# Kernel tuning notes

Hardware: AMD Instinct MI355X
Metric: run time of the kernel (lower is better)

Reference implementation:

```python
import jax, jax.numpy as jnp
import numpy as np

B, N, C = 32, 128, 128
HE = 64                      # n_hidden_edge
FILTERS = [64, 256, 512]
K = 3
NREL = 2
NH = 256                     # n_hidden
OUT = 10
EPS_BN = 1e-5


def _lin(key, fin, fout):
    return jax.random.normal(key, (fin, fout), jnp.float32) / np.sqrt(fin)


def setup_inputs() -> dict:
    key = jax.random.key(0)
    ks = iter(jax.random.split(key, 64))
    x = jax.random.normal(next(ks), (B, N, C), jnp.float32)
    # ragged mask: first n_b nodes active
    n_nodes = jax.random.randint(next(ks), (B,), 64, N + 1)
    mask = (jnp.arange(N)[None, :] < n_nodes[:, None]).astype(jnp.float32)
    A = jax.random.uniform(next(ks), (B, N, N), jnp.float32)
    A = A * mask[:, :, None] * mask[:, None, :]
    inp = {"x": x, "A": A, "mask": mask}
    # edge predictor MLP: Linear(2C,HE) -> ReLU -> Linear(HE,1)
    inp["eW1"] = _lin(next(ks), 2 * C, HE)
    inp["eb1"] = jnp.zeros((HE,), jnp.float32)
    inp["eW2"] = _lin(next(ks), HE, 1)
    inp["eb2"] = jnp.zeros((1,), jnp.float32)
    # 3 GraphConv layers: fc (in*K*NREL -> f), BN eval params
    fin = C
    for li, f in enumerate(FILTERS):
        inp[f"gW{li}"] = _lin(next(ks), fin * K * NREL, f)
        inp[f"gb{li}"] = jnp.zeros((f,), jnp.float32)
        inp[f"g{li}g"] = jnp.ones((f,), jnp.float32)
        inp[f"g{li}b"] = jnp.zeros((f,), jnp.float32)
        inp[f"g{li}m"] = 0.1 * jax.random.normal(next(ks), (f,), jnp.float32)
        inp[f"g{li}v"] = jax.random.uniform(next(ks), (f,), jnp.float32) + 0.5
        fin = f
    # classifier fc (dropout is identity in eval)
    inp["fW1"] = _lin(next(ks), FILTERS[-1], NH)
    inp["fb1"] = jnp.zeros((NH,), jnp.float32)
    inp["fW2"] = _lin(next(ks), NH, OUT)
    inp["fb2"] = jnp.zeros((OUT,), jnp.float32)
    return inp


def _edge_adjacency(x, mask, eW1, eb1, eW2, eb2):
    # edge_pred(cat(x_i,x_j)) for all pairs; flipped pass == transpose of scores
    u = x @ eW1[:C]          # [B,N,HE] (contribution of node i slot)
    v = x @ eW1[C:]          # [B,N,HE] (contribution of node j slot)
    h = jax.nn.relu(u[:, :, None, :] + v[:, None, :, :] + eb1)   # [B,N,N,HE]
    s = jnp.einsum('bijh,h->bij', h, eW2[:, 0]) + eb2[0]          # [B,N,N]
    y = jnp.exp(0.5 * (s + jnp.swapaxes(s, 1, 2)))
    # only masked upper-triangular pairs (i<j) were scattered in the original
    tri = jnp.triu(jnp.ones((N, N), bool), 1)
    pm = tri[None, :, :] * (mask[:, :, None] * mask[:, None, :])
    A_pred = y * pm
    rs = jnp.sum(A_pred, axis=2)                                 # row sums (torch sum over dim 1 of [N,N])
    rs = jnp.where(rs == 0.0, 1.0, rs)
    An = A_pred / rs[:, :, None]
    return An + jnp.swapaxes(An, 1, 2)


def _gconv(xh, A2, mask, W, b, g, be, m, v):
    outs = []
    for rel in range(A2.shape[-1]):
        Ar = A2[..., rel]
        # K>=2, scale_identity=False -> no identity added
        D = (jnp.sum(Ar, axis=1) + 1e-5) ** (-0.5)               # [B,N]
        L = D[:, :, None] * Ar * D[:, None, :]
        Xt = [xh, jnp.matmul(L, xh)]
        for _ in range(2, K):
            Xt.append(2.0 * jnp.matmul(L, Xt[-1]) - Xt[-2])
        outs.append(jnp.concatenate(Xt, axis=2))
    h = jnp.concatenate(outs, axis=2) @ W + b
    h = h * mask[:, :, None]
    h = (h - m) / jnp.sqrt(v + EPS_BN) * g + be                  # BatchNorm1d eval over channel dim
    return jax.nn.relu(h)


def reference(x, A, mask, eW1, eb1, eW2, eb2,
              gW0, gb0, g0g, g0b, g0m, g0v,
              gW1, gb1, g1g, g1b, g1m, g1v,
              gW2, gb2, g2g, g2b, g2m, g2v,
              fW1, fb1, fW2, fb2):
    An = _edge_adjacency(x, mask, eW1, eb1, eW2, eb2)
    A2 = jnp.stack((A, An), axis=3)                              # [B,N,N,2]
    h = _gconv(x, A2, mask, gW0, gb0, g0g, g0b, g0m, g0v)
    h = _gconv(h, A2, mask, gW1, gb1, g1g, g1b, g1m, g1v)
    h = _gconv(h, A2, mask, gW2, gb2, g2g, g2b, g2m, g2v)
    pooled = jnp.max(h, axis=1)                                  # [B, 512]
    # fc: Dropout(eval=id) -> Linear -> Dropout(eval=id) -> Linear (no activation)
    return (pooled @ fW1 + fb1) @ fW2 + fb2
```

## Files before the change

kernel.cpp:

```cpp
#include <hip/hip_runtime.h>

#define Bk 32
#define Nn 128
#define Cc 128
#define HE 64
#define BN_EPS 1e-5f

typedef __attribute__((ext_vector_type(8))) short short8;
typedef __attribute__((ext_vector_type(4))) float floatx4;

#define OFF_UV   ((size_t)0)
#define OFF_AP   ((size_t)524288)
#define OFF_LB   ((size_t)1048576)
#define OFF_H0   ((size_t)1572864)
#define OFF_H1   ((size_t)1835008)
#define OFF_POOL ((size_t)2883584)
#define OFF_WC   ((size_t)2899968)
#define OFF_BC   ((size_t)2905088)
#define OFF_XB0  ((size_t)2905104)
#define OFF_XB   ((size_t)3167248)
#define OFF_WT   ((size_t)6312976)
#define WUV_OFS  933888

__device__ __forceinline__ unsigned short f2b(float f) {
    unsigned int x = __float_as_uint(f);
    unsigned int r = x + 0x7FFFu + ((x >> 16) & 1u);
    return (unsigned short)(r >> 16);
}

__global__ __launch_bounds__(256) void prep_all(const float* __restrict__ W0,
                                                const float* __restrict__ W1,
                                                const float* __restrict__ W2,
                                                const float* __restrict__ eW1,
                                                const float* __restrict__ fW1,
                                                const float* __restrict__ fb1,
                                                const float* __restrict__ fW2,
                                                const float* __restrict__ fb2,
                                                const float* __restrict__ x,
                                                unsigned short* __restrict__ Wt,
                                                float* __restrict__ Wc,
                                                float* __restrict__ bc,
                                                unsigned short* __restrict__ xb0) {
    __shared__ unsigned short Ts[64][65];
    int bid = blockIdx.x, tid = threadIdx.x;
    if (bid < 228) {
        const float* src; unsigned short* dst; int N, ldK, k0, n0;
        if (bid < 12)      { src = W0; dst = Wt;          N = 64;  ldK = 768;  k0 = bid * 64;        n0 = 0; }
        else if (bid < 36) { int t = bid - 12; src = W1; dst = Wt + 49152;  N = 256; ldK = 384;  k0 = (t % 6) * 64;  n0 = (t / 6) * 64; }
        else               { int t = bid - 36; src = W2; dst = Wt + 147456; N = 512; ldK = 1536; k0 = (t % 24) * 64; n0 = (t / 24) * 64; }
#pragma unroll
        for (int p = 0; p < 16; ++p) {
            int e = tid + p * 256; int r = e >> 6, c = e & 63;
            Ts[r][c] = f2b(src[(size_t)(k0 + r) * N + n0 + c]);
        }
        __syncthreads();
#pragma unroll
        for (int p = 0; p < 16; ++p) {
            int e = tid + p * 256; int n = e >> 6, k = e & 63;
            dst[(size_t)(n0 + n) * ldK + k0 + k] = Ts[k][n];
        }
        return;
    }
    if (bid < 232) {
        int tt = bid - 228;
        int half = tt >> 1, kt = tt & 1;
        int k0 = kt * 64;
        unsigned short* Wuv = Wt + WUV_OFS;
#pragma unroll
        for (int p = 0; p < 16; ++p) {
            int e = tid + p * 256; int r = e >> 6, c = e & 63;
            Ts[r][c] = f2b(eW1[(size_t)(half * 128 + k0 + r) * 64 + c]);
        }
        __syncthreads();
#pragma unroll
        for (int p = 0; p < 16; ++p) {
            int e = tid + p * 256; int n = e >> 6, k = e & 63;
            Wuv[(size_t)(half * 64 + n) * 128 + k0 + k] = Ts[k][n];
        }
        return;
    }
    if (bid < 253) {
        int e = (bid - 232) * 256 + tid;
        if (e < 5120) {
            int i = e / 10, j = e - i * 10;
            float acc = 0.f;
            for (int h = 0; h < 256; ++h) acc += fW1[(size_t)i * 256 + h] * fW2[(size_t)h * 10 + j];
            Wc[e] = acc;
        } else if (e < 5130) {
            int j = e - 5120;
            float acc = fb2[j];
            for (int h = 0; h < 256; ++h) acc += fb1[h] * fW2[(size_t)h * 10 + j];
            bc[j] = acc;
        }
        return;
    }
    {
        int idx = (bid - 253) * 256 + tid;
        float4 vv = ((const float4*)x)[idx];
        ushort4 o;
        o.x = f2b(vv.x); o.y = f2b(vv.y); o.z = f2b(vv.z); o.w = f2b(vv.w);
        ((ushort4*)xb0)[idx] = o;
    }
}

__global__ __launch_bounds__(256) void uv_mfma(const unsigned short* __restrict__ xb0,
                                               const unsigned short* __restrict__ Wuv,
                                               const float* __restrict__ eb1,
                                               float* __restrict__ uv) {
    __shared__ __align__(16) unsigned short As[128 * 40];
    __shared__ __align__(16) unsigned short Bs[64 * 40];
    int tid = threadIdx.x;
    int w = tid >> 6, lane = tid & 63, quad = lane >> 4, lr = lane & 15;
    int row0 = blockIdx.y * 128, col0 = blockIdx.x * 64;
    floatx4 acc[2][4];
#pragma unroll
    for (int rt = 0; rt < 2; ++rt)
#pragma unroll
        for (int ct = 0; ct < 4; ++ct) acc[rt][ct] = (floatx4){0.f, 0.f, 0.f, 0.f};
    int arow[2], asub[2];
#pragma unroll
    for (int i = 0; i < 2; ++i) { int ch = tid + i * 256; arow[i] = ch >> 2; asub[i] = ch & 3; }
    int brow = tid >> 2, bsub = tid & 3;
    for (int k0 = 0; k0 < 128; k0 += 32) {
        short8 ra[2];
#pragma unroll
        for (int i = 0; i < 2; ++i)
            ra[i] = *(const short8*)(xb0 + (size_t)(row0 + arow[i]) * 128 + k0 + asub[i] * 8);
        short8 rb = *(const short8*)(Wuv + (size_t)(col0 + brow) * 128 + k0 + bsub * 8);
        __syncthreads();
#pragma unroll
        for (int i = 0; i < 2; ++i) *(short8*)&As[arow[i] * 40 + asub[i] * 8] = ra[i];
        *(short8*)&Bs[brow * 40 + bsub * 8] = rb;
        __syncthreads();
        short8 a[2], b[4];
#pragma unroll
        for (int rt = 0; rt < 2; ++rt)
            a[rt] = *(const short8*)&As[(w * 32 + rt * 16 + lr) * 40 + quad * 8];
#pragma unroll
        for (int ct = 0; ct < 4; ++ct)
            b[ct] = *(const short8*)&Bs[(ct * 16 + lr) * 40 + quad * 8];
#pragma unroll
        for (int rt = 0; rt < 2; ++rt)
#pragma unroll
            for (int ct = 0; ct < 4; ++ct)
                acc[rt][ct] = __builtin_amdgcn_mfma_f32_16x16x32_bf16(a[rt], b[ct], acc[rt][ct], 0, 0, 0);
    }
#pragma unroll
    for (int rt = 0; rt < 2; ++rt) {
        int rbase = row0 + w * 32 + rt * 16 + quad * 4;
#pragma unroll
        for (int ct = 0; ct < 4; ++ct) {
            int col = col0 + ct * 16 + lr;
            float bi = (col < 64) ? eb1[col] : 0.f;
#pragma unroll
            for (int reg = 0; reg < 4; ++reg)
                uv[(size_t)(rbase + reg) * 128 + col] = acc[rt][ct][reg] + bi;
        }
    }
}

__global__ __launch_bounds__(256) void edge_sym(const float* __restrict__ uv,
                                                const float* __restrict__ eW2,
                                                const float* __restrict__ eb2,
                                                const float* __restrict__ mask,
                                                float* __restrict__ ap) {
    __shared__ __align__(16) float ui[16][68], vi[16][68], uj[16][68], vj[16][68];
    __shared__ __align__(16) float w2[64];
    int t = blockIdx.x, b = blockIdx.y;
    int ti = 0, rem = t;
    for (;;) { int w = 8 - ti; if (rem < w) break; rem -= w; ++ti; }
    int tj = ti + rem;
    int i0 = ti * 16, j0 = tj * 16;
    int tid = threadIdx.x;
    int r = tid >> 4, c4 = (tid & 15) * 4;
    const float* uvb = uv + (size_t)b * Nn * 128;
    *(float4*)&ui[r][c4] = *(const float4*)(uvb + (size_t)(i0 + r) * 128 + c4);
    *(float4*)&vi[r][c4] = *(const float4*)(uvb + (size_t)(i0 + r) * 128 + 64 + c4);
    *(float4*)&uj[r][c4] = *(const float4*)(uvb + (size_t)(j0 + r) * 128 + c4);
    *(float4*)&vj[r][c4] = *(const float4*)(uvb + (size_t)(j0 + r) * 128 + 64 + c4);
    if (tid < 64) w2[tid] = eW2[tid];
    __syncthreads();
    int il = tid >> 4, jl = tid & 15;
    int gi = i0 + il, gj = j0 + jl;
    if (gj <= gi) return;
    float d = 0.f;
#pragma unroll
    for (int h4 = 0; h4 < 16; ++h4) {
        float4 a1 = *(const float4*)&ui[il][h4 * 4];
        float4 b1 = *(const float4*)&vj[jl][h4 * 4];
        float4 a2 = *(const float4*)&uj[jl][h4 * 4];
        float4 b2 = *(const float4*)&vi[il][h4 * 4];
        float4 ww = *(const float4*)&w2[h4 * 4];
        d += (fmaxf(a1.x + b1.x, 0.f) + fmaxf(a2.x + b2.x, 0.f)) * ww.x
           + (fmaxf(a1.y + b1.y, 0.f) + fmaxf(a2.y + b2.y, 0.f)) * ww.y
           + (fmaxf(a1.z + b1.z, 0.f) + fmaxf(a2.z + b2.z, 0.f)) * ww.z
           + (fmaxf(a1.w + b1.w, 0.f) + fmaxf(a2.w + b2.w, 0.f)) * ww.w;
    }
    float p = 0.5f * d + eb2[0];
    float mi = mask[b * Nn + gi], mj = mask[b * Nn + gj];
    float val = (mi != 0.f && mj != 0.f) ? expf(fminf(p, 80.f)) : 0.f;
    ap[((size_t)(b * Nn + gi)) * Nn + gj] = val;
}

__global__ __launch_bounds__(256) void adj_L(const float* __restrict__ ap,
                                             const float* __restrict__ A,
                                             unsigned short* __restrict__ Lb) {
    int bid = blockIdx.x, tid = threadIdx.x;
    if (bid < 32) {
        int b = bid;
        __shared__ float apS[128][129];
        __shared__ float part[256], invS[128], t1S[128], Dv[128];
        const float* apg = ap + (size_t)b * Nn * Nn;
        for (int k = 0; k < 64; ++k) {
            int idx = tid + k * 256;
            int i = idx >> 7, j = idx & 127;
            float g = apg[idx];
            apS[i][j] = (j > i) ? g : 0.f;
        }
        __syncthreads();
        {
            int row = tid >> 1, half = tid & 1;
            float s0 = 0.f;
            for (int j = half * 64; j < half * 64 + 64; ++j) s0 += apS[row][j];
            part[tid] = s0;
        }
        __syncthreads();
        if (tid < 128) {
            float rsum = part[tid * 2] + part[tid * 2 + 1];
            invS[tid] = (rsum == 0.f) ? 1.f : (1.f / rsum);
            t1S[tid]  = (rsum == 0.f) ? 0.f : 1.f;
        }
        __syncthreads();
        {
            int col = tid >> 1, half = tid & 1;
            float s0 = 0.f;
            for (int j = half * 64; j < half * 64 + 64; ++j) s0 += apS[j][col] * invS[j];
            part[tid] = s0;
        }
        __syncthreads();
        if (tid < 128) Dv[tid] = rsqrtf(t1S[tid] + part[tid * 2] + part[tid * 2 + 1] + 1e-5f);
        __syncthreads();
        unsigned short* Lo = Lb + ((size_t)(Bk + b)) * Nn * Nn;
        for (int k = 0; k < 64; ++k) {
            int idx = tid + k * 256;
            int i = idx >> 7, j = idx & 127;
            float an = apS[i][j] * invS[i] + apS[j][i] * invS[j];
            Lo[idx] = f2b(Dv[i] * an * Dv[j]);
        }
    } else {
        int b = bid - 32;
        const float* Ar = A + (size_t)b * Nn * Nn;
        __shared__ float part2[256];
        __shared__ float Ds[128];
        int j = tid & 127, half = tid >> 7;
        float sum = 0.f;
        for (int i = half * 64; i < half * 64 + 64; ++i) sum += Ar[i * Nn + j];
        part2[tid] = sum;
        __syncthreads();
        if (tid < 128) Ds[tid] = rsqrtf(part2[tid] + part2[tid + 128] + 1e-5f);
        __syncthreads();
        unsigned short* Lo = Lb + (size_t)b * Nn * Nn;
        for (int k = 0; k < 64; ++k) {
            int idx = tid + k * 256;
            int i = idx >> 7, jj = idx & 127;
            Lo[idx] = f2b(Ds[i] * Ar[idx] * Ds[jj]);
        }
    }
}

template <int FIN, int COLS>
__global__ __launch_bounds__(256) void cheb_fused(const unsigned short* __restrict__ Lb,
                                                  const float* __restrict__ xin,
                                                  unsigned short* __restrict__ Xb) {
    constexpr int LDK = 136;
    constexpr int NCT = COLS / 16;
    constexpr int HC  = COLS / 2;
    __shared__ __align__(16) unsigned short Ls[128 * LDK];
    __shared__ __align__(16) unsigned short XsT[COLS * LDK];
    __shared__ __align__(16) unsigned short T1T[COLS * LDK];
    int z = blockIdx.y;
    int b = z & 31, rel = z >> 5;
    int c0 = blockIdx.x * COLS;
    int tid = threadIdx.x;
    int w = tid >> 6, lane = tid & 63, quad = lane >> 4, lr = lane & 15;
    const unsigned short* Lp = Lb + ((size_t)(rel * Bk + b)) * Nn * Nn;
    const float* Xp = xin + (size_t)b * Nn * FIN;
    const int ld6 = 6 * FIN;
    unsigned short* Xo = Xb + (size_t)b * Nn * ld6 + rel * 3 * FIN;

#pragma unroll
    for (int i = 0; i < 16; ++i) {
        int idx = tid + i * 256;
        int row = idx >> 5, col4 = (idx & 31) << 2;
        ushort4 val = *(const ushort4*)(Lp + row * Nn + col4);
        *(ushort4*)&Ls[row * LDK + col4] = val;
    }
    {
        int node = tid >> 1, cb = (tid & 1) * HC;
        const float* xr = Xp + (size_t)node * FIN + c0 + cb;
        unsigned short* t0w = Xo + (size_t)node * ld6 + c0 + cb;
#pragma unroll
        for (int i = 0; i < HC / 4; ++i) {
            float4 vv = *(const float4*)(xr + i * 4);
            ushort4 o;
            o.x = f2b(vv.x); o.y = f2b(vv.y); o.z = f2b(vv.z); o.w = f2b(vv.w);
            *(ushort4*)(t0w + i * 4) = o;
            XsT[(cb + i * 4 + 0) * LDK + node] = o.x;
            XsT[(cb + i * 4 + 1) * LDK + node] = o.y;
            XsT[(cb + i * 4 + 2) * LDK + node] = o.z;
            XsT[(cb + i * 4 + 3) * LDK + node] = o.w;
        }
    }
    __syncthreads();

    floatx4 acc[2][NCT];
#pragma unroll
    for (int rt = 0; rt < 2; ++rt)
#pragma unroll
        for (int ct = 0; ct < NCT; ++ct) acc[rt][ct] = (floatx4){0.f, 0.f, 0.f, 0.f};
#pragma unroll
    for (int kc = 0; kc < 4; ++kc) {
        short8 a[2], bb[NCT];
#pragma unroll
        for (int rt = 0; rt < 2; ++rt)
            a[rt] = *(const short8*)&Ls[((w * 2 + rt) * 16 + lr) * LDK + kc * 32 + quad * 8];
#pragma unroll
        for (int ct = 0; ct < NCT; ++ct)
            bb[ct] = *(const short8*)&XsT[(ct * 16 + lr) * LDK + kc * 32 + quad * 8];
#pragma unroll
        for (int rt = 0; rt < 2; ++rt)
#pragma unroll
            for (int ct = 0; ct < NCT; ++ct)
                acc[rt][ct] = __builtin_amdgcn_mfma_f32_16x16x32_bf16(a[rt], bb[ct], acc[rt][ct], 0, 0, 0);
    }
#pragma unroll
    for (int rt = 0; rt < 2; ++rt) {
        int rb = (w * 2 + rt) * 16 + quad * 4;
#pragma unroll
        for (int ct = 0; ct < NCT; ++ct) {
            int col = ct * 16 + lr;
            ushort4 o;
            o.x = f2b(acc[rt][ct][0]); o.y = f2b(acc[rt][ct][1]);
            o.z = f2b(acc[rt][ct][2]); o.w = f2b(acc[rt][ct][3]);
            *(ushort4*)&T1T[col * LDK + rb] = o;
        }
    }
    __syncthreads();
    {
        int node = tid >> 1, cb = (tid & 1) * HC;
        unsigned short* t1w = Xo + (size_t)node * ld6 + FIN + c0 + cb;
#pragma unroll
        for (int i = 0; i < HC / 4; ++i) {
            ushort4 o;
            o.x = T1T[(cb + i * 4 + 0) * LDK + node];
            o.y = T1T[(cb + i * 4 + 1) * LDK + node];
            o.z = T1T[(cb + i * 4 + 2) * LDK + node];
            o.w = T1T[(cb + i * 4 + 3) * LDK + node];
            *(ushort4*)(t1w + i * 4) = o;
        }
    }
    floatx4 acc2[2][NCT];
#pragma unroll
    for (int rt = 0; rt < 2; ++rt)
#pragma unroll
        for (int ct = 0; ct < NCT; ++ct) acc2[rt][ct] = (floatx4){0.f, 0.f, 0.f, 0.f};
#pragma unroll
    for (int kc = 0; kc < 4; ++kc) {
        short8 a[2], bb[NCT];
#pragma unroll
        for (int rt = 0; rt < 2; ++rt)
            a[rt] = *(const short8*)&Ls[((w * 2 + rt) * 16 + lr) * LDK + kc * 32 + quad * 8];
#pragma unroll
        for (int ct = 0; ct < NCT; ++ct)
            bb[ct] = *(const short8*)&T1T[(ct * 16 + lr) * LDK + kc * 32 + quad * 8];
#pragma unroll
        for (int rt = 0; rt < 2; ++rt)
#pragma unroll
            for (int ct = 0; ct < NCT; ++ct)
                acc2[rt][ct] = __builtin_amdgcn_mfma_f32_16x16x32_bf16(a[rt], bb[ct], acc2[rt][ct], 0, 0, 0);
    }
#pragma unroll
    for (int rt = 0; rt < 2; ++rt) {
        int rb = (w * 2 + rt) * 16 + quad * 4;
#pragma unroll
        for (int ct = 0; ct < NCT; ++ct) {
            int col = ct * 16 + lr;
            ushort4 o;
            float t0a = Xp[(size_t)(rb + 0) * FIN + c0 + col];
            float t0b = Xp[(size_t)(rb + 1) * FIN + c0 + col];
            float t0c = Xp[(size_t)(rb + 2) * FIN + c0 + col];
            float t0d = Xp[(size_t)(rb + 3) * FIN + c0 + col];
            o.x = f2b(2.f * acc2[rt][ct][0] - t0a);
            o.y = f2b(2.f * acc2[rt][ct][1] - t0b);
            o.z = f2b(2.f * acc2[rt][ct][2] - t0c);
            o.w = f2b(2.f * acc2[rt][ct][3] - t0d);
            *(ushort4*)&XsT[col * LDK + rb] = o;
        }
    }
    __syncthreads();
    {
        int node = tid >> 1, cb = (tid & 1) * HC;
        unsigned short* t2w = Xo + (size_t)node * ld6 + 2 * FIN + c0 + cb;
#pragma unroll
        for (int i = 0; i < HC / 4; ++i) {
            ushort4 o;
            o.x = XsT[(cb + i * 4 + 0) * LDK + node];
            o.y = XsT[(cb + i * 4 + 1) * LDK + node];
            o.z = XsT[(cb + i * 4 + 2) * LDK + node];
            o.w = XsT[(cb + i * 4 + 3) * LDK + node];
            *(ushort4*)(t2w + i * 4) = o;
        }
    }
}

template <int RT, bool POOL>
__global__ __launch_bounds__(256) void fc_mfma(const unsigned short* __restrict__ Xb,
                                               const unsigned short* __restrict__ Wt,
                                               const float* __restrict__ bias,
                                               const float* __restrict__ mask,
                                               const float* __restrict__ bnG,
                                               const float* __restrict__ bnB,
                                               const float* __restrict__ bnM,
                                               const float* __restrict__ bnV,
                                               float* __restrict__ out,
                                               float* __restrict__ pooled,
                                               int Kd, int F) {
    __shared__ __align__(16) unsigned short As[RT * 64 * 40];
    __shared__ __align__(16) unsigned short Bs[64 * 40];
    __shared__ float wmax[4][64];
    int tid = threadIdx.x;
    int w = tid >> 6, lane = tid & 63, quad = lane >> 4, lr = lane & 15;
    int row0 = blockIdx.y * (RT * 64), col0 = blockIdx.x * 64;

    floatx4 acc[RT][4];
#pragma unroll
    for (int rt = 0; rt < RT; ++rt)
#pragma unroll
        for (int ct = 0; ct < 4; ++ct) acc[rt][ct] = (floatx4){0.f, 0.f, 0.f, 0.f};

    int arow[RT], asub[RT];
#pragma unroll
    for (int i = 0; i < RT; ++i) { int ch = tid + i * 256; arow[i] = ch >> 2; asub[i] = ch & 3; }
    int brow = tid >> 2, bsub = tid & 3;

    for (int k0 = 0; k0 < Kd; k0 += 32) {
        short8 ra[RT];
#pragma unroll
        for (int i = 0; i < RT; ++i)
            ra[i] = *(const short8*)(Xb + (size_t)(row0 + arow[i]) * Kd + k0 + asub[i] * 8);
        short8 rb = *(const short8*)(Wt + (size_t)(col0 + brow) * Kd + k0 + bsub * 8);
        __syncthreads();
#pragma unroll
        for (int i = 0; i < RT; ++i)
            *(short8*)&As[arow[i] * 40 + asub[i] * 8] = ra[i];
        *(short8*)&Bs[brow * 40 + bsub * 8] = rb;
        __syncthreads();
        short8 a[RT], b[4];
#pragma unroll
        for (int rt = 0; rt < RT; ++rt)
            a[rt] = *(const short8*)&As[(w * RT * 16 + rt * 16 + lr) * 40 + quad * 8];
#pragma unroll
        for (int ct = 0; ct < 4; ++ct)
            b[ct] = *(const short8*)&Bs[(ct * 16 + lr) * 40 + quad * 8];
#pragma unroll
        for (int rt = 0; rt < RT; ++rt)
#pragma unroll
            for (int ct = 0; ct < 4; ++ct)
                acc[rt][ct] = __builtin_amdgcn_mfma_f32_16x16x32_bf16(a[rt], b[ct], acc[rt][ct], 0, 0, 0);
    }

    float cm[4] = {0.f, 0.f, 0.f, 0.f};
#pragma unroll
    for (int rt = 0; rt < RT; ++rt) {
        int rbase = row0 + w * RT * 16 + rt * 16 + quad * 4;
#pragma unroll
        for (int ct = 0; ct < 4; ++ct) {
            int col = col0 + ct * 16 + lr;
            float bi = bias[col];
            float sc = rsqrtf(bnV[col] + BN_EPS) * bnG[col];
            float bm = bnM[col], bb = bnB[col];
#pragma unroll
            for (int reg = 0; reg < 4; ++reg) {
                int row = rbase + reg;
                float h = acc[rt][ct][reg] + bi;
                h *= mask[row];
                h = (h - bm) * sc + bb;
                h = fmaxf(h, 0.f);
                if (POOL) cm[ct] = fmaxf(cm[ct], h);
                else      out[(size_t)row * F + col] = h;
            }
        }
    }
    if (POOL) {
#pragma unroll
        for (int ct = 0; ct < 4; ++ct) {
            cm[ct] = fmaxf(cm[ct], __shfl_xor(cm[ct], 16));
            cm[ct] = fmaxf(cm[ct], __shfl_xor(cm[ct], 32));
            if (quad == 0) wmax[w][ct * 16 + lr] = cm[ct];
        }
        __syncthreads();
        if (tid < 64) {
            float g = fmaxf(fmaxf(wmax[0][tid], wmax[1][tid]), fmaxf(wmax[2][tid], wmax[3][tid]));
            int b = blockIdx.y;
            pooled[(size_t)b * 512 + col0 + tid] = g;
        }
    }
}

__global__ __launch_bounds__(256) void cls_final(const float* __restrict__ pooled,
                                                 const float* __restrict__ Wc,
                                                 const float* __restrict__ bc,
                                                 float* __restrict__ out) {
    __shared__ float red[16][17];
    int b = blockIdx.x, tid = threadIdx.x;
    int o = tid & 15, slice = tid >> 4;
    float p = 0.f;
    if (o < 10) {
        for (int kk = 0; kk < 32; ++kk) {
            int k = slice * 32 + kk;
            p += pooled[(size_t)b * 512 + k] * Wc[(size_t)k * 10 + o];
        }
    }
    red[slice][o] = p;
    __syncthreads();
    if (tid < 10) {
        float sum = bc[tid];
        for (int sli = 0; sli < 16; ++sli) sum += red[sli][tid];
        out[(size_t)b * 10 + tid] = sum;
    }
}

extern "C" void kernel_launch(void* const* d_in, const int* in_sizes, int n_in,
                              void* d_out, int out_size, void* d_ws, size_t ws_size,
                              hipStream_t stream) {
    const float* x    = (const float*)d_in[0];
    const float* Ain  = (const float*)d_in[1];
    const float* mask = (const float*)d_in[2];
    const float* eW1  = (const float*)d_in[3];
    const float* eb1  = (const float*)d_in[4];
    const float* eW2  = (const float*)d_in[5];
    const float* eb2  = (const float*)d_in[6];
    const float* fW1  = (const float*)d_in[25];
    const float* fb1  = (const float*)d_in[26];
    const float* fW2  = (const float*)d_in[27];
    const float* fb2  = (const float*)d_in[28];

    float* ws = (float*)d_ws;
    float* uv = ws + OFF_UV;
    float* ap = ws + OFF_AP;
    unsigned short* Lb = (unsigned short*)(ws + OFF_LB);
    float* h0 = ws + OFF_H0;
    float* h1 = ws + OFF_H1;
    float* pl = ws + OFF_POOL;
    float* Wc = ws + OFF_WC;
    float* bc = ws + OFF_BC;
    unsigned short* xb0 = (unsigned short*)(ws + OFF_XB0);
    unsigned short* Xb  = (unsigned short*)(ws + OFF_XB);
    unsigned short* Wt  = (unsigned short*)(ws + OFF_WT);

    prep_all<<<765, 256, 0, stream>>>((const float*)d_in[7], (const float*)d_in[13],
                                      (const float*)d_in[19], eW1, fW1, fb1, fW2, fb2, x,
                                      Wt, Wc, bc, xb0);

    uv_mfma<<<dim3(2, 32), 256, 0, stream>>>(xb0, Wt + WUV_OFS, eb1, uv);
    edge_sym<<<dim3(36, Bk), 256, 0, stream>>>(uv, eW2, eb2, mask, ap);
    adj_L<<<64, 256, 0, stream>>>(ap, Ain, Lb);

    const float* xins[3] = {x, h0, h1};
    const unsigned short* Wts[3] = {Wt, Wt + 49152, Wt + 147456};
    const int Kds[3] = {768, 384, 1536};
    for (int li = 0; li < 3; ++li) {
        int base = 7 + li * 6;
        const float* gb = (const float*)d_in[base + 1];
        const float* gg = (const float*)d_in[base + 2];
        const float* gB = (const float*)d_in[base + 3];
        const float* gm = (const float*)d_in[base + 4];
        const float* gv = (const float*)d_in[base + 5];

        if (li == 0)      cheb_fused<128, 32><<<dim3(4, 64), 256, 0, stream>>>(Lb, xins[li], Xb);
        else if (li == 1) cheb_fused<64, 32><<<dim3(2, 64), 256, 0, stream>>>(Lb, xins[li], Xb);
        else              cheb_fused<256, 32><<<dim3(8, 64), 256, 0, stream>>>(Lb, xins[li], Xb);

        if (li == 0)
            fc_mfma<1, false><<<dim3(1, 64), 256, 0, stream>>>(
                Xb, Wts[li], gb, mask, gg, gB, gm, gv, h0, nullptr, Kds[li], 64);
        else if (li == 1)
            fc_mfma<2, false><<<dim3(4, 32), 256, 0, stream>>>(
                Xb, Wts[li], gb, mask, gg, gB, gm, gv, h1, nullptr, Kds[li], 256);
        else
            fc_mfma<2, true><<<dim3(8, 32), 256, 0, stream>>>(
                Xb, Wts[li], gb, mask, gg, gB, gm, gv, nullptr, pl, Kds[li], 512);
    }

    cls_final<<<Bk, 256, 0, stream>>>(pl, Wc, bc, (float*)d_out);
}
```

Baseline: 231.2 us.

## Precompute 2L^2-I per graph so Chebyshev terms compute in parallel

The adjacency kernel now also builds M = 2·L·L − I in bf16 with MFMA for each batch and relation, and writes it to a new workspace buffer. The Chebyshev kernel then gets T1 = L·X and T2 = M·X from one pass over X, instead of chaining T2 = 2·L·T1 − X. This drops a synchronisation and the dependent second GEMM, along with the global reloads of X, in each of the three layers. In exchange it adds L² work once, doubles the L-matrix bytes each cheb block loads, raises shared memory use, and changes rounding because T2 no longer comes from the rounded T1.

```diff
diff --git a/kernel.cpp b/kernel.cpp
--- a/kernel.cpp
+++ b/kernel.cpp
@@ -20,6 +20,7 @@
 #define OFF_XB0  ((size_t)2905104)
 #define OFF_XB   ((size_t)3167248)
 #define OFF_WT   ((size_t)6312976)
+#define OFF_L2M  ((size_t)6788112)
 #define WUV_OFS  933888
 
 __device__ __forceinline__ unsigned short f2b(float f) {
@@ -202,14 +203,20 @@
     ap[((size_t)(b * Nn + gi)) * Nn + gj] = val;
 }
 
-__global__ __launch_bounds__(256) void adj_L(const float* __restrict__ ap,
-                                             const float* __restrict__ A,
-                                             unsigned short* __restrict__ Lb) {
+__global__ __launch_bounds__(256) void adj_L2(const float* __restrict__ ap,
+                                              const float* __restrict__ A,
+                                              unsigned short* __restrict__ Lb,
+                                              unsigned short* __restrict__ L2m) {
+    __shared__ float apS[128][129];
+    __shared__ __align__(16) unsigned short LbS[128 * 136];
+    __shared__ __align__(16) unsigned short LbT[128 * 136];
+    __shared__ float part[256];
+    __shared__ float sc1[128], t1S[128], sc2[128];
     int bid = blockIdx.x, tid = threadIdx.x;
+    int w = tid >> 6, lane = tid & 63, quad = lane >> 4, lr = lane & 15;
+    int rel, b;
     if (bid < 32) {
-        int b = bid;
-        __shared__ float apS[128][129];
-        __shared__ float part[256], invS[128], t1S[128], Dv[128];
+        rel = 1; b = bid;
         const float* apg = ap + (size_t)b * Nn * Nn;
         for (int k = 0; k < 64; ++k) {
             int idx = tid + k * 256;
@@ -227,63 +234,114 @@
         __syncthreads();
         if (tid < 128) {
             float rsum = part[tid * 2] + part[tid * 2 + 1];
-            invS[tid] = (rsum == 0.f) ? 1.f : (1.f / rsum);
-            t1S[tid]  = (rsum == 0.f) ? 0.f : 1.f;
+            sc1[tid] = (rsum == 0.f) ? 1.f : (1.f / rsum);
+            t1S[tid] = (rsum == 0.f) ? 0.f : 1.f;
         }
         __syncthreads();
         {
             int col = tid >> 1, half = tid & 1;
             float s0 = 0.f;
-            for (int j = half * 64; j < half * 64 + 64; ++j) s0 += apS[j][col] * invS[j];
+            for (int j = half * 64; j < half * 64 + 64; ++j) s0 += apS[j][col] * sc1[j];
             part[tid] = s0;
         }
         __syncthreads();
-        if (tid < 128) Dv[tid] = rsqrtf(t1S[tid] + part[tid * 2] + part[tid * 2 + 1] + 1e-5f);
+        if (tid < 128) sc2[tid] = rsqrtf(t1S[tid] + part[tid * 2] + part[tid * 2 + 1] + 1e-5f);
         __syncthreads();
         unsigned short* Lo = Lb + ((size_t)(Bk + b)) * Nn * Nn;
         for (int k = 0; k < 64; ++k) {
             int idx = tid + k * 256;
             int i = idx >> 7, j = idx & 127;
-            float an = apS[i][j] * invS[i] + apS[j][i] * invS[j];
-            Lo[idx] = f2b(Dv[i] * an * Dv[j]);
+            float an = apS[i][j] * sc1[i] + apS[j][i] * sc1[j];
+            unsigned short hv = f2b(sc2[i] * an * sc2[j]);
+            LbS[i * 136 + j] = hv;
+            Lo[idx] = hv;
         }
     } else {
-        int b = bid - 32;
+        rel = 0; b = bid - 32;
         const float* Ar = A + (size_t)b * Nn * Nn;
-        __shared__ float part2[256];
-        __shared__ float Ds[128];
-        int j = tid & 127, half = tid >> 7;
-        float sum = 0.f;
-        for (int i = half * 64; i < half * 64 + 64; ++i) sum += Ar[i * Nn + j];
-        part2[tid] = sum;
-        __syncthreads();
-        if (tid < 128) Ds[tid] = rsqrtf(part2[tid] + part2[tid + 128] + 1e-5f);
+        {
+            int j = tid & 127, half = tid >> 7;
+            float sum = 0.f;
+            for (int i = half * 64; i < half * 64 + 64; ++i) sum += Ar[i * Nn + j];
+            part[tid] = sum;
+        }
+        __syncthreads();
+        if (tid < 128) sc2[tid] = rsqrtf(part[tid] + part[tid + 128] + 1e-5f);
         __syncthreads();
         unsigned short* Lo = Lb + (size_t)b * Nn * Nn;
         for (int k = 0; k < 64; ++k) {
             int idx = tid + k * 256;
-            int i = idx >> 7, jj = idx & 127;
-            Lo[idx] = f2b(Ds[i] * Ar[idx] * Ds[jj]);
-        }
-    }
-}
-
-template <int FIN, int COLS>
-__global__ __launch_bounds__(256) void cheb_fused(const unsigned short* __restrict__ Lb,
-                                                  const float* __restrict__ xin,
-                                                  unsigned short* __restrict__ Xb) {
+            int i = idx >> 7, j = idx & 127;
+            unsigned short hv = f2b(sc2[i] * Ar[idx] * sc2[j]);
+            LbS[i * 136 + j] = hv;
+            LbT[j * 136 + i] = hv;
+            Lo[idx] = hv;
+        }
+    }
+    __syncthreads();
+    const unsigned short* Bsrc = (bid < 32) ? LbS : LbT;
+    floatx4 acc[2][8];
+#pragma unroll
+    for (int rt = 0; rt < 2; ++rt)
+#pragma unroll
+        for (int ct = 0; ct < 8; ++ct) acc[rt][ct] = (floatx4){0.f, 0.f, 0.f, 0.f};
+#pragma unroll
+    for (int kc = 0; kc < 4; ++kc) {
+        short8 a[2], bb[8];
+#pragma unroll
+        for (int rt = 0; rt < 2; ++rt)
+            a[rt] = *(const short8*)&LbS[((w * 2 + rt) * 16 + lr) * 136 + kc * 32 + quad * 8];
+#pragma unroll
+        for (int ct = 0; ct < 8; ++ct)
+            bb[ct] = *(const short8*)&Bsrc[(ct * 16 + lr) * 136 + kc * 32 + quad * 8];
+#pragma unroll
+        for (int rt = 0; rt < 2; ++rt)
+#pragma unroll
+            for (int ct = 0; ct < 8; ++ct)
+                acc[rt][ct] = __builtin_amdgcn_mfma_f32_16x16x32_bf16(a[rt], bb[ct], acc[rt][ct], 0, 0, 0);
+    }
+    unsigned short* stage = (unsigned short*)&apS[0][0];
+#pragma unroll
+    for (int rt = 0; rt < 2; ++rt) {
+        int rb = w * 32 + rt * 16 + quad * 4;
+#pragma unroll
+        for (int ct = 0; ct < 8; ++ct) {
+            int col = ct * 16 + lr;
+#pragma unroll
+            for (int reg = 0; reg < 4; ++reg) {
+                int row = rb + reg;
+                stage[row * 136 + col] = f2b(2.f * acc[rt][ct][reg] - ((row == col) ? 1.f : 0.f));
+            }
+        }
+    }
+    __syncthreads();
+    unsigned short* Mo = L2m + ((size_t)(rel * Bk + b)) * Nn * Nn;
+#pragma unroll
+    for (int i = 0; i < 16; ++i) {
+        int idx = tid + i * 256;
+        int row = idx >> 5, c4 = (idx & 31) << 2;
+        *(ushort4*)(Mo + row * Nn + c4) = *(ushort4*)&stage[row * 136 + c4];
+    }
+}
+
+template <int FIN>
+__global__ __launch_bounds__(256) void cheb_v2(const unsigned short* __restrict__ Lb,
+                                               const unsigned short* __restrict__ L2m,
+                                               const float* __restrict__ xin,
+                                               unsigned short* __restrict__ Xb) {
     constexpr int LDK = 136;
-    constexpr int NCT = COLS / 16;
-    constexpr int HC  = COLS / 2;
     __shared__ __align__(16) unsigned short Ls[128 * LDK];
-    __shared__ __align__(16) unsigned short XsT[COLS * LDK];
-    __shared__ __align__(16) unsigned short T1T[COLS * LDK];
+    __shared__ __align__(16) unsigned short L2s[128 * LDK];
+    __shared__ __align__(16) unsigned short XsT[32 * LDK];
+    __shared__ __align__(16) unsigned short T1T[32 * LDK];
+    __shared__ __align__(16) unsigned short T2T[32 * LDK];
     int z = blockIdx.y;
     int b = z & 31, rel = z >> 5;
-    int c0 = blockIdx.x * COLS;
+    int c0 = blockIdx.x * 32;
     int tid = threadIdx.x;
     int w = tid >> 6, lane = tid & 63, quad = lane >> 4, lr = lane & 15;
-    const unsigned short* Lp = Lb + ((size_t)(rel * Bk + b)) * Nn * Nn;
+    const unsigned short* Lp  = Lb  + ((size_t)(rel * Bk + b)) * Nn * Nn;
+    const unsigned short* L2p = L2m + ((size_t)(rel * Bk + b)) * Nn * Nn;
     const float* Xp = xin + (size_t)b * Nn * FIN;
     const int ld6 = 6 * FIN;
     unsigned short* Xo = Xb + (size_t)b * Nn * ld6 + rel * 3 * FIN;
@@ -292,15 +350,15 @@
     for (int i = 0; i < 16; ++i) {
         int idx = tid + i * 256;
         int row = idx >> 5, col4 = (idx & 31) << 2;
-        ushort4 val = *(const ushort4*)(Lp + row * Nn + col4);
-        *(ushort4*)&Ls[row * LDK + col4] = val;
+        *(ushort4*)&Ls[row * LDK + col4]  = *(const ushort4*)(Lp  + row * Nn + col4);
+        *(ushort4*)&L2s[row * LDK + col4] = *(const ushort4*)(L2p + row * Nn + col4);
     }
     {
-        int node = tid >> 1, cb = (tid & 1) * HC;
+        int node = tid >> 1, cb = (tid & 1) * 16;
         const float* xr = Xp + (size_t)node * FIN + c0 + cb;
         unsigned short* t0w = Xo + (size_t)node * ld6 + c0 + cb;
 #pragma unroll
-        for (int i = 0; i < HC / 4; ++i) {
+        for (int i = 0; i < 4; ++i) {
             float4 vv = *(const float4*)(xr + i * 4);
             ushort4 o;
             o.x = f2b(vv.x); o.y = f2b(vv.y); o.z = f2b(vv.z); o.w = f2b(vv.w);
@@ -313,102 +371,66 @@
     }
     __syncthreads();
 
-    floatx4 acc[2][NCT];
+    floatx4 acc1[2][2], acc2[2][2];
 #pragma unroll
     for (int rt = 0; rt < 2; ++rt)
 #pragma unroll
-        for (int ct = 0; ct < NCT; ++ct) acc[rt][ct] = (floatx4){0.f, 0.f, 0.f, 0.f};
+        for (int ct = 0; ct < 2; ++ct) {
+            acc1[rt][ct] = (floatx4){0.f, 0.f, 0.f, 0.f};
+            acc2[rt][ct] = (floatx4){0.f, 0.f, 0.f, 0.f};
+        }
 #pragma unroll
     for (int kc = 0; kc < 4; ++kc) {
-        short8 a[2], bb[NCT];
+        short8 a1[2], a2[2], bb[2];
+#pragma unroll
+        for (int rt = 0; rt < 2; ++rt) {
+            a1[rt] = *(const short8*)&Ls[((w * 2 + rt) * 16 + lr) * LDK + kc * 32 + quad * 8];
+            a2[rt] = *(const short8*)&L2s[((w * 2 + rt) * 16 + lr) * LDK + kc * 32 + quad * 8];
+        }
+#pragma unroll
+        for (int ct = 0; ct < 2; ++ct)
+            bb[ct] = *(const short8*)&XsT[(ct * 16 + lr) * LDK + kc * 32 + quad * 8];
 #pragma unroll
         for (int rt = 0; rt < 2; ++rt)
-            a[rt] = *(const short8*)&Ls[((w * 2 + rt) * 16 + lr) * LDK + kc * 32 + quad * 8];
-#pragma unroll
-        for (int ct = 0; ct < NCT; ++ct)
-            bb[ct] = *(const short8*)&XsT[(ct * 16 + lr) * LDK + kc * 32 + quad * 8];
-#pragma unroll
-        for (int rt = 0; rt < 2; ++rt)
-#pragma unroll
-            for (int ct = 0; ct < NCT; ++ct)
-                acc[rt][ct] = __builtin_amdgcn_mfma_f32_16x16x32_bf16(a[rt], bb[ct], acc[rt][ct], 0, 0, 0);
+#pragma unroll
+            for (int ct = 0; ct < 2; ++ct) {
+                acc1[rt][ct] = __builtin_amdgcn_mfma_f32_16x16x32_bf16(a1[rt], bb[ct], acc1[rt][ct], 0, 0, 0);
+                acc2[rt][ct] = __builtin_amdgcn_mfma_f32_16x16x32_bf16(a2[rt], bb[ct], acc2[rt][ct], 0, 0, 0);
+            }
     }
 #pragma unroll
     for (int rt = 0; rt < 2; ++rt) {
         int rb = (w * 2 + rt) * 16 + quad * 4;
 #pragma unroll
-        for (int ct = 0; ct < NCT; ++ct) {
+        for (int ct = 0; ct < 2; ++ct) {
             int col = ct * 16 + lr;
-            ushort4 o;
-            o.x = f2b(acc[rt][ct][0]); o.y = f2b(acc[rt][ct][1]);
-            o.z = f2b(acc[rt][ct][2]); o.w = f2b(acc[rt][ct][3]);
-            *(ushort4*)&T1T[col * LDK + rb] = o;
+            ushort4 o1, o2;
+            o1.x = f2b(acc1[rt][ct][0]); o1.y = f2b(acc1[rt][ct][1]);
+            o1.z = f2b(acc1[rt][ct][2]); o1.w = f2b(acc1[rt][ct][3]);
+            o2.x = f2b(acc2[rt][ct][0]); o2.y = f2b(acc2[rt][ct][1]);
+            o2.z = f2b(acc2[rt][ct][2]); o2.w = f2b(acc2[rt][ct][3]);
+            *(ushort4*)&T1T[col * LDK + rb] = o1;
+            *(ushort4*)&T2T[col * LDK + rb] = o2;
         }
     }
     __syncthreads();
     {
-        int node = tid >> 1, cb = (tid & 1) * HC;
+        int node = tid >> 1, cb = (tid & 1) * 16;
         unsigned short* t1w = Xo + (size_t)node * ld6 + FIN + c0 + cb;
-#pragma unroll
-        for (int i = 0; i < HC / 4; ++i) {
-            ushort4 o;
-            o.x = T1T[(cb + i * 4 + 0) * LDK + node];
-            o.y = T1T[(cb + i * 4 + 1) * LDK + node];
-            o.z = T1T[(cb + i * 4 + 2) * LDK + node];
-            o.w = T1T[(cb + i * 4 + 3) * LDK + node];
-            *(ushort4*)(t1w + i * 4) = o;
-        }
-    }
-    floatx4 acc2[2][NCT];
-#pragma unroll
-    for (int rt = 0; rt < 2; ++rt)
-#pragma unroll
-        for (int ct = 0; ct < NCT; ++ct) acc2[rt][ct] = (floatx4){0.f, 0.f, 0.f, 0.f};
-#pragma unroll
-    for (int kc = 0; kc < 4; ++kc) {
-        short8 a[2], bb[NCT];
-#pragma unroll
-        for (int rt = 0; rt < 2; ++rt)
-            a[rt] = *(const short8*)&Ls[((w * 2 + rt) * 16 + lr) * LDK + kc * 32 + quad * 8];
-#pragma unroll
-        for (int ct = 0; ct < NCT; ++ct)
-            bb[ct] = *(const short8*)&T1T[(ct * 16 + lr) * LDK + kc * 32 + quad * 8];
-#pragma unroll
-        for (int rt = 0; rt < 2; ++rt)
-#pragma unroll
-            for (int ct = 0; ct < NCT; ++ct)
-                acc2[rt][ct] = __builtin_amdgcn_mfma_f32_16x16x32_bf16(a[rt], bb[ct], acc2[rt][ct], 0, 0, 0);
-    }
-#pragma unroll
-    for (int rt = 0; rt < 2; ++rt) {
-        int rb = (w * 2 + rt) * 16 + quad * 4;
-#pragma unroll
-        for (int ct = 0; ct < NCT; ++ct) {
-            int col = ct * 16 + lr;
-            ushort4 o;
-            float t0a = Xp[(size_t)(rb + 0) * FIN + c0 + col];
-            float t0b = Xp[(size_t)(rb + 1) * FIN + c0 + col];
-            float t0c = Xp[(size_t)(rb + 2) * FIN + c0 + col];
-            float t0d = Xp[(size_t)(rb + 3) * FIN + c0 + col];
-            o.x = f2b(2.f * acc2[rt][ct][0] - t0a);
-            o.y = f2b(2.f * acc2[rt][ct][1] - t0b);
-            o.z = f2b(2.f * acc2[rt][ct][2] - t0c);
-            o.w = f2b(2.f * acc2[rt][ct][3] - t0d);
-            *(ushort4*)&XsT[col * LDK + rb] = o;
-        }
-    }
-    __syncthreads();
-    {
-        int node = tid >> 1, cb = (tid & 1) * HC;
         unsigned short* t2w = Xo + (size_t)node * ld6 + 2 * FIN + c0 + cb;
 #pragma unroll
-        for (int i = 0; i < HC / 4; ++i) {
-            ushort4 o;
-            o.x = XsT[(cb + i * 4 + 0) * LDK + node];
-            o.y = XsT[(cb + i * 4 + 1) * LDK + node];
-            o.z = XsT[(cb + i * 4 + 2) * LDK + node];
-            o.w = XsT[(cb + i * 4 + 3) * LDK + node];
-            *(ushort4*)(t2w + i * 4) = o;
+        for (int i = 0; i < 4; ++i) {
+            ushort4 o1, o2;
+            o1.x = T1T[(cb + i * 4 + 0) * LDK + node];
+            o1.y = T1T[(cb + i * 4 + 1) * LDK + node];
+            o1.z = T1T[(cb + i * 4 + 2) * LDK + node];
+            o1.w = T1T[(cb + i * 4 + 3) * LDK + node];
+            o2.x = T2T[(cb + i * 4 + 0) * LDK + node];
+            o2.y = T2T[(cb + i * 4 + 1) * LDK + node];
+            o2.z = T2T[(cb + i * 4 + 2) * LDK + node];
+            o2.w = T2T[(cb + i * 4 + 3) * LDK + node];
+            *(ushort4*)(t1w + i * 4) = o1;
+            *(ushort4*)(t2w + i * 4) = o2;
         }
     }
 }
@@ -548,7 +570,8 @@
     float* ws = (float*)d_ws;
     float* uv = ws + OFF_UV;
     float* ap = ws + OFF_AP;
-    unsigned short* Lb = (unsigned short*)(ws + OFF_LB);
+    unsigned short* Lb  = (unsigned short*)(ws + OFF_LB);
+    unsigned short* L2m = (unsigned short*)(ws + OFF_L2M);
     float* h0 = ws + OFF_H0;
     float* h1 = ws + OFF_H1;
     float* pl = ws + OFF_POOL;
@@ -564,7 +587,7 @@
 
     uv_mfma<<<dim3(2, 32), 256, 0, stream>>>(xb0, Wt + WUV_OFS, eb1, uv);
     edge_sym<<<dim3(36, Bk), 256, 0, stream>>>(uv, eW2, eb2, mask, ap);
-    adj_L<<<64, 256, 0, stream>>>(ap, Ain, Lb);
+    adj_L2<<<64, 256, 0, stream>>>(ap, Ain, Lb, L2m);
 
     const float* xins[3] = {x, h0, h1};
     const unsigned short* Wts[3] = {Wt, Wt + 49152, Wt + 147456};
@@ -577,9 +600,9 @@
         const float* gm = (const float*)d_in[base + 4];
         const float* gv = (const float*)d_in[base + 5];
 
-        if (li == 0)      cheb_fused<128, 32><<<dim3(4, 64), 256, 0, stream>>>(Lb, xins[li], Xb);
-        else if (li == 1) cheb_fused<64, 32><<<dim3(2, 64), 256, 0, stream>>>(Lb, xins[li], Xb);
-        else              cheb_fused<256, 32><<<dim3(8, 64), 256, 0, stream>>>(Lb, xins[li], Xb);
+        if (li == 0)      cheb_v2<128><<<dim3(4, 64), 256, 0, stream>>>(Lb, L2m, xins[li], Xb);
+        else if (li == 1) cheb_v2<64><<<dim3(2, 64), 256, 0, stream>>>(Lb, L2m, xins[li], Xb);
+        else              cheb_v2<256><<<dim3(8, 64), 256, 0, stream>>>(Lb, L2m, xins[li], Xb);
 
         if (li == 0)
             fc_mfma<1, false><<<dim3(1, 64), 256, 0, stream>>>(
```

New measurement: 245.1 us. 6.0% more time.

## Hold Laplacian A-fragments in registers and fuse classifier into last FC via atomics

Applied to the files above, without the earlier changes.

The Chebyshev kernel no longer stages the full 128x128 Laplacian tile in LDS. Each wave loads its own A-operand fragments straight from global memory into registers and reuses them for both MFMA passes, which cuts LDS footprint and one copy pass and should raise occupancy. The final classifier matmul moves into the pooling epilogue of the last FC kernel, using wave shuffles plus atomicAdd into a pre-zeroed output. This removes the cls_final launch and the pooled buffer, but adds a memset and nondeterministic float atomic accumulation.

```diff
diff --git a/kernel.cpp b/kernel.cpp
--- a/kernel.cpp
+++ b/kernel.cpp
@@ -14,7 +14,6 @@
 #define OFF_LB   ((size_t)1048576)
 #define OFF_H0   ((size_t)1572864)
 #define OFF_H1   ((size_t)1835008)
-#define OFF_POOL ((size_t)2883584)
 #define OFF_WC   ((size_t)2899968)
 #define OFF_BC   ((size_t)2905088)
 #define OFF_XB0  ((size_t)2905104)
@@ -268,19 +267,16 @@
     }
 }
 
-template <int FIN, int COLS>
-__global__ __launch_bounds__(256) void cheb_fused(const unsigned short* __restrict__ Lb,
-                                                  const float* __restrict__ xin,
-                                                  unsigned short* __restrict__ Xb) {
+template <int FIN>
+__global__ __launch_bounds__(256) void cheb_v4(const unsigned short* __restrict__ Lb,
+                                               const float* __restrict__ xin,
+                                               unsigned short* __restrict__ Xb) {
     constexpr int LDK = 136;
-    constexpr int NCT = COLS / 16;
-    constexpr int HC  = COLS / 2;
-    __shared__ __align__(16) unsigned short Ls[128 * LDK];
-    __shared__ __align__(16) unsigned short XsT[COLS * LDK];
-    __shared__ __align__(16) unsigned short T1T[COLS * LDK];
+    __shared__ __align__(16) unsigned short XsT[32 * LDK];
+    __shared__ __align__(16) unsigned short T1T[32 * LDK];
     int z = blockIdx.y;
     int b = z & 31, rel = z >> 5;
-    int c0 = blockIdx.x * COLS;
+    int c0 = blockIdx.x * 32;
     int tid = threadIdx.x;
     int w = tid >> 6, lane = tid & 63, quad = lane >> 4, lr = lane & 15;
     const unsigned short* Lp = Lb + ((size_t)(rel * Bk + b)) * Nn * Nn;
@@ -288,19 +284,20 @@
     const int ld6 = 6 * FIN;
     unsigned short* Xo = Xb + (size_t)b * Nn * ld6 + rel * 3 * FIN;
 
-#pragma unroll
-    for (int i = 0; i < 16; ++i) {
-        int idx = tid + i * 256;
-        int row = idx >> 5, col4 = (idx & 31) << 2;
-        ushort4 val = *(const ushort4*)(Lp + row * Nn + col4);
-        *(ushort4*)&Ls[row * LDK + col4] = val;
+    short8 aL[2][4];
+#pragma unroll
+    for (int rt = 0; rt < 2; ++rt) {
+        int row = w * 32 + rt * 16 + lr;
+#pragma unroll
+        for (int kc = 0; kc < 4; ++kc)
+            aL[rt][kc] = *(const short8*)(Lp + (size_t)row * Nn + kc * 32 + quad * 8);
     }
     {
-        int node = tid >> 1, cb = (tid & 1) * HC;
+        int node = tid >> 1, cb = (tid & 1) * 16;
         const float* xr = Xp + (size_t)node * FIN + c0 + cb;
         unsigned short* t0w = Xo + (size_t)node * ld6 + c0 + cb;
 #pragma unroll
-        for (int i = 0; i < HC / 4; ++i) {
+        for (int i = 0; i < 4; ++i) {
             float4 vv = *(const float4*)(xr + i * 4);
             ushort4 o;
             o.x = f2b(vv.x); o.y = f2b(vv.y); o.z = f2b(vv.z); o.w = f2b(vv.w);
@@ -313,44 +310,42 @@
     }
     __syncthreads();
 
-    floatx4 acc[2][NCT];
+    floatx4 acc1[2][2];
 #pragma unroll
     for (int rt = 0; rt < 2; ++rt)
 #pragma unroll
-        for (int ct = 0; ct < NCT; ++ct) acc[rt][ct] = (floatx4){0.f, 0.f, 0.f, 0.f};
+        for (int ct = 0; ct < 2; ++ct) acc1[rt][ct] = (floatx4){0.f, 0.f, 0.f, 0.f};
 #pragma unroll
     for (int kc = 0; kc < 4; ++kc) {
-        short8 a[2], bb[NCT];
+        short8 bb[2];
+#pragma unroll
+        for (int ct = 0; ct < 2; ++ct)
+            bb[ct] = *(const short8*)&XsT[(ct * 16 + lr) * LDK + kc * 32 + quad * 8];
 #pragma unroll
         for (int rt = 0; rt < 2; ++rt)
-            a[rt] = *(const short8*)&Ls[((w * 2 + rt) * 16 + lr) * LDK + kc * 32 + quad * 8];
-#pragma unroll
-        for (int ct = 0; ct < NCT; ++ct)
-            bb[ct] = *(const short8*)&XsT[(ct * 16 + lr) * LDK + kc * 32 + quad * 8];
-#pragma unroll
-        for (int rt = 0; rt < 2; ++rt)
-#pragma unroll
-            for (int ct = 0; ct < NCT; ++ct)
-                acc[rt][ct] = __builtin_amdgcn_mfma_f32_16x16x32_bf16(a[rt], bb[ct], acc[rt][ct], 0, 0, 0);
+#pragma unroll
+            for (int ct = 0; ct < 2; ++ct)
+                acc1[rt][ct] = __builtin_amdgcn_mfma_f32_16x16x32_bf16(aL[rt][kc], bb[ct], acc1[rt][ct], 0, 0, 0);
     }
 #pragma unroll
     for (int rt = 0; rt < 2; ++rt) {
         int rb = (w * 2 + rt) * 16 + quad * 4;
 #pragma unroll
-        for (int ct = 0; ct < NCT; ++ct) {
+        for (int ct = 0; ct < 2; ++ct) {
             int col = ct * 16 + lr;
             ushort4 o;
-            o.x = f2b(acc[rt][ct][0]); o.y = f2b(acc[rt][ct][1]);
-            o.z = f2b(acc[rt][ct][2]); o.w = f2b(acc[rt][ct][3]);
+            o.x = f2b(acc1[rt][ct][0]); o.y = f2b(acc1[rt][ct][1]);
+            o.z = f2b(acc1[rt][ct][2]); o.w = f2b(acc1[rt][ct][3]);
             *(ushort4*)&T1T[col * LDK + rb] = o;
         }
     }
     __syncthreads();
+
     {
-        int node = tid >> 1, cb = (tid & 1) * HC;
+        int node = tid >> 1, cb = (tid & 1) * 16;
         unsigned short* t1w = Xo + (size_t)node * ld6 + FIN + c0 + cb;
 #pragma unroll
-        for (int i = 0; i < HC / 4; ++i) {
+        for (int i = 0; i < 4; ++i) {
             ushort4 o;
             o.x = T1T[(cb + i * 4 + 0) * LDK + node];
             o.y = T1T[(cb + i * 4 + 1) * LDK + node];
@@ -359,31 +354,28 @@
             *(ushort4*)(t1w + i * 4) = o;
         }
     }
-    floatx4 acc2[2][NCT];
+    floatx4 acc2[2][2];
 #pragma unroll
     for (int rt = 0; rt < 2; ++rt)
 #pragma unroll
-        for (int ct = 0; ct < NCT; ++ct) acc2[rt][ct] = (floatx4){0.f, 0.f, 0.f, 0.f};
+        for (int ct = 0; ct < 2; ++ct) acc2[rt][ct] = (floatx4){0.f, 0.f, 0.f, 0.f};
 #pragma unroll
     for (int kc = 0; kc < 4; ++kc) {
-        short8 a[2], bb[NCT];
+        short8 bb[2];
+#pragma unroll
+        for (int ct = 0; ct < 2; ++ct)
+            bb[ct] = *(const short8*)&T1T[(ct * 16 + lr) * LDK + kc * 32 + quad * 8];
 #pragma unroll
         for (int rt = 0; rt < 2; ++rt)
-            a[rt] = *(const short8*)&Ls[((w * 2 + rt) * 16 + lr) * LDK + kc * 32 + quad * 8];
-#pragma unroll
-        for (int ct = 0; ct < NCT; ++ct)
-            bb[ct] = *(const short8*)&T1T[(ct * 16 + lr) * LDK + kc * 32 + quad * 8];
-#pragma unroll
-        for (int rt = 0; rt < 2; ++rt)
-#pragma unroll
-            for (int ct = 0; ct < NCT; ++ct)
-                acc2[rt][ct] = __builtin_amdgcn_mfma_f32_16x16x32_bf16(a[rt], bb[ct], acc2[rt][ct], 0, 0, 0);
+#pragma unroll
+            for (int ct = 0; ct < 2; ++ct)
+                acc2[rt][ct] = __builtin_amdgcn_mfma_f32_16x16x32_bf16(aL[rt][kc], bb[ct], acc2[rt][ct], 0, 0, 0);
     }
 #pragma unroll
     for (int rt = 0; rt < 2; ++rt) {
         int rb = (w * 2 + rt) * 16 + quad * 4;
 #pragma unroll
-        for (int ct = 0; ct < NCT; ++ct) {
+        for (int ct = 0; ct < 2; ++ct) {
             int col = ct * 16 + lr;
             ushort4 o;
             float t0a = Xp[(size_t)(rb + 0) * FIN + c0 + col];
@@ -399,10 +391,10 @@
     }
     __syncthreads();
     {
-        int node = tid >> 1, cb = (tid & 1) * HC;
+        int node = tid >> 1, cb = (tid & 1) * 16;
         unsigned short* t2w = Xo + (size_t)node * ld6 + 2 * FIN + c0 + cb;
 #pragma unroll
-        for (int i = 0; i < HC / 4; ++i) {
+        for (int i = 0; i < 4; ++i) {
             ushort4 o;
             o.x = XsT[(cb + i * 4 + 0) * LDK + node];
             o.y = XsT[(cb + i * 4 + 1) * LDK + node];
@@ -423,7 +415,9 @@
                                                const float* __restrict__ bnM,
                                                const float* __restrict__ bnV,
                                                float* __restrict__ out,
-                                               float* __restrict__ pooled,
+                                               const float* __restrict__ Wc,
+                                               const float* __restrict__ bc,
+                                               float* __restrict__ outc,
                                                int Kd, int F) {
     __shared__ __align__(16) unsigned short As[RT * 64 * 40];
     __shared__ __align__(16) unsigned short Bs[64 * 40];
@@ -501,32 +495,22 @@
         __syncthreads();
         if (tid < 64) {
             float g = fmaxf(fmaxf(wmax[0][tid], wmax[1][tid]), fmaxf(wmax[2][tid], wmax[3][tid]));
-            int b = blockIdx.y;
-            pooled[(size_t)b * 512 + col0 + tid] = g;
-        }
-    }
-}
-
-__global__ __launch_bounds__(256) void cls_final(const float* __restrict__ pooled,
-                                                 const float* __restrict__ Wc,
-                                                 const float* __restrict__ bc,
-                                                 float* __restrict__ out) {
-    __shared__ float red[16][17];
-    int b = blockIdx.x, tid = threadIdx.x;
-    int o = tid & 15, slice = tid >> 4;
-    float p = 0.f;
-    if (o < 10) {
-        for (int kk = 0; kk < 32; ++kk) {
-            int k = slice * 32 + kk;
-            p += pooled[(size_t)b * 512 + k] * Wc[(size_t)k * 10 + o];
-        }
-    }
-    red[slice][o] = p;
-    __syncthreads();
-    if (tid < 10) {
-        float sum = bc[tid];
-        for (int sli = 0; sli < 16; ++sli) sum += red[sli][tid];
-        out[(size_t)b * 10 + tid] = sum;
+            float s[10];
+#pragma unroll
+            for (int o = 0; o < 10; ++o) s[o] = g * Wc[(size_t)(col0 + tid) * 10 + o];
+#pragma unroll
+            for (int ofs = 32; ofs > 0; ofs >>= 1)
+#pragma unroll
+                for (int o = 0; o < 10; ++o) s[o] += __shfl_down(s[o], ofs);
+            if (tid == 0) {
+                int b = blockIdx.y;
+#pragma unroll
+                for (int o = 0; o < 10; ++o) {
+                    float v = s[o] + ((blockIdx.x == 0) ? bc[o] : 0.f);
+                    atomicAdd(&outc[b * 10 + o], v);
+                }
+            }
+        }
     }
 }
 
@@ -551,12 +535,13 @@
     unsigned short* Lb = (unsigned short*)(ws + OFF_LB);
     float* h0 = ws + OFF_H0;
     float* h1 = ws + OFF_H1;
-    float* pl = ws + OFF_POOL;
     float* Wc = ws + OFF_WC;
     float* bc = ws + OFF_BC;
     unsigned short* xb0 = (unsigned short*)(ws + OFF_XB0);
     unsigned short* Xb  = (unsigned short*)(ws + OFF_XB);
     unsigned short* Wt  = (unsigned short*)(ws + OFF_WT);
+
+    hipMemsetAsync(d_out, 0, (size_t)out_size * sizeof(float), stream);
 
     prep_all<<<765, 256, 0, stream>>>((const float*)d_in[7], (const float*)d_in[13],
                                       (const float*)d_in[19], eW1, fW1, fb1, fW2, fb2, x,
@@ -577,20 +562,18 @@
         const float* gm = (const float*)d_in[base + 4];
         const float* gv = (const float*)d_in[base + 5];
 
-        if (li == 0)      cheb_fused<128, 32><<<dim3(4, 64), 256, 0, stream>>>(Lb, xins[li], Xb);
-        else if (li == 1) cheb_fused<64, 32><<<dim3(2, 64), 256, 0, stream>>>(Lb, xins[li], Xb);
-        else              cheb_fused<256, 32><<<dim3(8, 64), 256, 0, stream>>>(Lb, xins[li], Xb);
+        if (li == 0)      cheb_v4<128><<<dim3(4, 64), 256, 0, stream>>>(Lb, xins[li], Xb);
+        else if (li == 1) cheb_v4<64><<<dim3(2, 64), 256, 0, stream>>>(Lb, xins[li], Xb);
+        else              cheb_v4<256><<<dim3(8, 64), 256, 0, stream>>>(Lb, xins[li], Xb);
 
         if (li == 0)
             fc_mfma<1, false><<<dim3(1, 64), 256, 0, stream>>>(
-                Xb, Wts[li], gb, mask, gg, gB, gm, gv, h0, nullptr, Kds[li], 64);
+                Xb, Wts[li], gb, mask, gg, gB, gm, gv, h0, nullptr, nullptr, nullptr, Kds[li], 64);
         else if (li == 1)
             fc_mfma<2, false><<<dim3(4, 32), 256, 0, stream>>>(
-                Xb, Wts[li], gb, mask, gg, gB, gm, gv, h1, nullptr, Kds[li], 256);
+                Xb, Wts[li], gb, mask, gg, gB, gm, gv, h1, nullptr, nullptr, nullptr, Kds[li], 256);
         else
             fc_mfma<2, true><<<dim3(8, 32), 256, 0, stream>>>(
-                Xb, Wts[li], gb, mask, gg, gB, gm, gv, nullptr, pl, Kds[li], 512);
-    }
-
-    cls_final<<<Bk, 256, 0, stream>>>(pl, Wc, bc, (float*)d_out);
-}
+                Xb, Wts[li], gb, mask, gg, gB, gm, gv, nullptr, Wc, bc, (float*)d_out, Kds[li], 512);
+    }
+}
```

Result: no change. 230.3 us (-0.4%).
